# Optimization experiments

Hardware: AMD Instinct MI355X
Metric: run time of the kernel (lower is better)

The kernel has to match this reference:

```python
import jax, jax.numpy as jnp
import numpy as np

def setup_inputs() -> dict:
    key = jax.random.key(0)
    kq, kk, kv = jax.random.split(key, 3)
    S, D = 4096, 512
    q = jax.random.normal(kq, (S, D), dtype=jnp.float32)
    k = jax.random.normal(kk, (S, D), dtype=jnp.float32)
    v = jax.random.normal(kv, (S, D), dtype=jnp.float32)
    return {"q": q, "k": k, "v": v}

def reference(q, k, v):
    # scaled dot-product attention, unmasked (mask_future=False path)
    d = q.shape[-1]
    scores = jnp.einsum('sd,td->st', q, k) / jnp.sqrt(jnp.asarray(d, q.dtype))
    attn = jax.nn.softmax(scores, axis=-1)
    return jnp.einsum('st,td->sd', attn, v)
```

## Files before the change

kernel.cpp:

```cpp
#include <hip/hip_runtime.h>
#include <hip/hip_bf16.h>

#define SEQ 4096
#define DIM 512
#define SCALE 0.044194173824159216f

#define SPLITS 4
#define BQ 64
#define KVBLK 64
#define KEYS_PER_SPLIT (SEQ / SPLITS)
#define ITERS (KEYS_PER_SPLIT / KVBLK)

typedef __attribute__((ext_vector_type(8))) short short8;
typedef __attribute__((ext_vector_type(4))) float f32x4;

__device__ __forceinline__ short f2bf(float f) {
  union { float f; unsigned u; } c; c.f = f;
  unsigned u = c.u;
  return (short)((u + 0x7FFFu + ((u >> 16) & 1u)) >> 16);
}

__device__ __forceinline__ short8 pack8(float4 a, float4 b) {
  short8 r;
  r[0] = f2bf(a.x); r[1] = f2bf(a.y); r[2] = f2bf(a.z); r[3] = f2bf(a.w);
  r[4] = f2bf(b.x); r[5] = f2bf(b.y); r[6] = f2bf(b.z); r[7] = f2bf(b.w);
  return r;
}

__device__ __forceinline__ void gload16(const void* g, void* l) {
  __builtin_amdgcn_global_load_lds(
      (const __attribute__((address_space(1))) unsigned int*)g,
      (__attribute__((address_space(3))) unsigned int*)l, 16, 0, 0);
}

__global__ void cvt_bf16(const float* __restrict__ in, ushort* __restrict__ ob, int n8) {
  int i = blockIdx.x * blockDim.x + threadIdx.x;
  if (i >= n8) return;
  const float4* p = (const float4*)(in + (size_t)i * 8);
  short8 v = pack8(p[0], p[1]);
  *(short8*)(ob + (size_t)i * 8) = v;
}

__global__ void transpose_bf16(const float* __restrict__ v, ushort* __restrict__ vt) {
  __shared__ float t[64][65];
  const int bs = blockIdx.x % (SEQ / 64);
  const int bd = blockIdx.x / (SEQ / 64);
  const int s0 = bs * 64, d0 = bd * 64;
  const int tid = threadIdx.x;
#pragma unroll
  for (int k = 0; k < 16; ++k) {
    int idx = k * 256 + tid;
    int r = idx >> 6, c = idx & 63;
    t[r][c] = v[(size_t)(s0 + r) * DIM + d0 + c];
  }
  __syncthreads();
#pragma unroll
  for (int k = 0; k < 16; ++k) {
    int idx = k * 256 + tid;
    int dr = idx >> 6, sc = idx & 63;
    vt[(size_t)(d0 + dr) * SEQ + s0 + sc] = (ushort)f2bf(t[sc][dr]);
  }
}

__global__ __launch_bounds__(512) void attn_split(
    const float* __restrict__ q, const ushort* __restrict__ kbf,
    const ushort* __restrict__ vt, float* __restrict__ opart,
    float* __restrict__ ml) {
  __shared__ __align__(16) ushort kt[KVBLK * DIM];
  __shared__ __align__(16) ushort vtt[DIM * KVBLK];
  __shared__ float s_lds[BQ][68];
  __shared__ __align__(16) ushort p_lds[BQ * KVBLK];
  __shared__ float m_st[BQ], l_st[BQ], osc_st[BQ];

  const int tid  = threadIdx.x;
  const int lane = tid & 63;
  const int w    = tid >> 6;
  const int lr   = lane & 15;
  const int lg   = lane >> 4;
  const int sp   = blockIdx.x & (SPLITS - 1);
  const int qb   = blockIdx.x >> 2;
  const int rg   = w & 3;
  const int g2   = w >> 2;
  const int qrow0 = qb * BQ;
  const int kbase = sp * KEYS_PER_SPLIT;

  if (tid < BQ) { m_st[tid] = -INFINITY; l_st[tid] = 0.f; }

  short8 qf[16];
  {
    const float* qp = q + (size_t)(qrow0 + rg * 16 + lr) * DIM + lg * 8;
#pragma unroll
    for (int c = 0; c < 16; ++c)
      qf[c] = pack8(*(const float4*)(qp + c * 32), *(const float4*)(qp + c * 32 + 4));
  }
  f32x4 oacc[16] = {};

  auto stageK = [&](int kb) {
#pragma unroll
    for (int i = 0; i < 8; ++i) {
      int r = w * 8 + i;
      const ushort* src = kbf + (size_t)(kb + r) * DIM + ((lane ^ (r & 31)) * 8);
      gload16(src, &kt[r * DIM]);
    }
  };
  auto stageV = [&](int kb) {
#pragma unroll
    for (int j = 0; j < 8; ++j) {
      int r0 = w * 64 + j * 8;
      int rr = r0 + (lane >> 3);
      int c  = lane & 7;
      const ushort* src = vt + (size_t)rr * SEQ + kb + ((c ^ (rr & 7)) * 8);
      gload16(src, &vtt[r0 * KVBLK]);
    }
  };

  stageK(kbase);

  for (int it = 0; it < ITERS; ++it) {
    const int kb = kbase + it * KVBLK;

    stageV(kb);
    asm volatile("s_waitcnt vmcnt(8)" ::: "memory");
    __builtin_amdgcn_s_barrier();

    {
      f32x4 s0 = {}, s1 = {};
      const int r0 = g2 * 32 + lr;
      const int r1 = r0 + 16;
      const char* ktb = (const char*)kt;
#pragma unroll
      for (int c = 0; c < 16; ++c) {
        short8 k0 = *(const short8*)(ktb + r0 * 1024 + (((c * 4 + lg) ^ (r0 & 31)) * 16));
        short8 k1 = *(const short8*)(ktb + r1 * 1024 + (((c * 4 + lg) ^ (r1 & 31)) * 16));
        s0 = __builtin_amdgcn_mfma_f32_16x16x32_bf16(qf[c], k0, s0, 0, 0, 0);
        s1 = __builtin_amdgcn_mfma_f32_16x16x32_bf16(qf[c], k1, s1, 0, 0, 0);
      }
#pragma unroll
      for (int r = 0; r < 4; ++r) {
        s_lds[rg * 16 + lg * 4 + r][g2 * 32 + lr]      = s0[r] * SCALE;
        s_lds[rg * 16 + lg * 4 + r][g2 * 32 + 16 + lr] = s1[r] * SCALE;
      }
    }
    asm volatile("s_waitcnt lgkmcnt(0)" ::: "memory");
    __builtin_amdgcn_s_barrier();

    {
      const int srow = tid >> 3;
      const int sj   = (tid & 7) * 8;
      float4 a = *(const float4*)&s_lds[srow][sj];
      float4 b = *(const float4*)&s_lds[srow][sj + 4];
      float tmax = fmaxf(fmaxf(fmaxf(a.x, a.y), fmaxf(a.z, a.w)),
                         fmaxf(fmaxf(b.x, b.y), fmaxf(b.z, b.w)));
#pragma unroll
      for (int m = 1; m <= 4; m <<= 1) tmax = fmaxf(tmax, __shfl_xor(tmax, m));
      float mold = m_st[srow];
      float mnew = fmaxf(mold, tmax);
      float p0 = __expf(a.x - mnew), p1 = __expf(a.y - mnew);
      float p2 = __expf(a.z - mnew), p3 = __expf(a.w - mnew);
      float p4 = __expf(b.x - mnew), p5 = __expf(b.y - mnew);
      float p6 = __expf(b.z - mnew), p7 = __expf(b.w - mnew);
      float ps = ((p0 + p1) + (p2 + p3)) + ((p4 + p5) + (p6 + p7));
#pragma unroll
      for (int m = 1; m <= 4; m <<= 1) ps += __shfl_xor(ps, m);
      if ((tid & 7) == 0) {
        float sc = __expf(mold - mnew);
        osc_st[srow] = sc;
        l_st[srow] = l_st[srow] * sc + ps;
        m_st[srow] = mnew;
      }
      short8 pb;
      pb[0] = f2bf(p0); pb[1] = f2bf(p1); pb[2] = f2bf(p2); pb[3] = f2bf(p3);
      pb[4] = f2bf(p4); pb[5] = f2bf(p5); pb[6] = f2bf(p6); pb[7] = f2bf(p7);
      int ba = srow * 128 + ((sj * 2) ^ ((srow & 7) << 4));
      *(short8*)((char*)p_lds + ba) = pb;
    }

    if (it + 1 < ITERS) stageK(kb + KVBLK);

    asm volatile("s_waitcnt vmcnt(8)" ::: "memory");
    asm volatile("s_waitcnt lgkmcnt(0)" ::: "memory");
    __builtin_amdgcn_s_barrier();

    {
      float osc[4];
#pragma unroll
      for (int r = 0; r < 4; ++r) osc[r] = osc_st[rg * 16 + lg * 4 + r];
#pragma unroll
      for (int ct = 0; ct < 16; ++ct)
#pragma unroll
        for (int r = 0; r < 4; ++r) oacc[ct][r] *= osc[r];

      const char* vb = (const char*)vtt;
#pragma unroll
      for (int kc = 0; kc < 2; ++kc) {
        const int prow = rg * 16 + lr;
        int ba = prow * 128 + ((kc * 64 + lg * 16) ^ ((prow & 7) << 4));
        short8 pf = *(const short8*)((const char*)p_lds + ba);
#pragma unroll
        for (int ct = 0; ct < 16; ++ct) {
          int drow = g2 * 256 + ct * 16 + lr;
          short8 vf = *(const short8*)(vb + drow * 128 + (((kc * 4 + lg) ^ (drow & 7)) * 16));
          oacc[ct] = __builtin_amdgcn_mfma_f32_16x16x32_bf16(pf, vf, oacc[ct], 0, 0, 0);
        }
      }
    }
    asm volatile("s_waitcnt lgkmcnt(0)" ::: "memory");
    __builtin_amdgcn_s_barrier();
  }

  {
    float* op = opart + ((size_t)sp * SEQ + qrow0 + rg * 16) * DIM + g2 * 256;
#pragma unroll
    for (int ct = 0; ct < 16; ++ct)
#pragma unroll
      for (int r = 0; r < 4; ++r)
        op[(size_t)(lg * 4 + r) * DIM + ct * 16 + lr] = oacc[ct][r];
    if (tid < BQ) {
      size_t base = ((size_t)sp * SEQ + qrow0 + tid) * 2;
      ml[base]     = m_st[tid];
      ml[base + 1] = l_st[tid];
    }
  }
}

__global__ void combine(const float* __restrict__ opart, const float* __restrict__ ml,
                        float* __restrict__ out) {
  int gid = blockIdx.x * 256 + threadIdx.x;
  int row = gid >> 7;
  int dv  = (gid & 127) * 4;
  float m[SPLITS], l[SPLITS], wgt[SPLITS];
  float M = -INFINITY;
#pragma unroll
  for (int i = 0; i < SPLITS; ++i) {
    m[i] = ml[((size_t)i * SEQ + row) * 2];
    l[i] = ml[((size_t)i * SEQ + row) * 2 + 1];
    M = fmaxf(M, m[i]);
  }
  float L = 0.f;
#pragma unroll
  for (int i = 0; i < SPLITS; ++i) { wgt[i] = __expf(m[i] - M); L += l[i] * wgt[i]; }
  float inv = 1.f / L;
  float4 acc = {0.f, 0.f, 0.f, 0.f};
#pragma unroll
  for (int i = 0; i < SPLITS; ++i) {
    float4 o = *(const float4*)(opart + ((size_t)i * SEQ + row) * DIM + dv);
    acc.x += o.x * wgt[i]; acc.y += o.y * wgt[i];
    acc.z += o.z * wgt[i]; acc.w += o.w * wgt[i];
  }
  acc.x *= inv; acc.y *= inv; acc.z *= inv; acc.w *= inv;
  *(float4*)(out + (size_t)row * DIM + dv) = acc;
}

__global__ __launch_bounds__(512) void attn_fused_fb(
    const float* __restrict__ q, const float* __restrict__ k,
    const float* __restrict__ v, float* __restrict__ out) {
  __shared__ float s_lds[16][128];
  __shared__ __align__(16) unsigned short p_lds[16 * 128];
  __shared__ float m_st[16], l_st[16], osc_st[16];
  const int tid = threadIdx.x, lane = tid & 63, w = tid >> 6;
  const int lr = lane & 15, lg = lane >> 4, qb = blockIdx.x * 16;
  if (tid < 16) { m_st[tid] = -INFINITY; l_st[tid] = 0.f; }
  short8 qf[16];
  {
    const float* qp = q + (size_t)(qb + lr) * DIM + lg * 8;
#pragma unroll
    for (int c = 0; c < 16; ++c)
      qf[c] = pack8(*(const float4*)(qp + c * 32), *(const float4*)(qp + c * 32 + 4));
  }
  f32x4 oacc[4] = {};
  __syncthreads();
  for (int it = 0; it < SEQ / 128; ++it) {
    const int kb = it * 128;
    {
      const float* kp = k + (size_t)(kb + w * 16 + lr) * DIM + lg * 8;
      f32x4 sacc = {};
#pragma unroll
      for (int c = 0; c < 16; ++c) {
        short8 kf = pack8(*(const float4*)(kp + c * 32), *(const float4*)(kp + c * 32 + 4));
        sacc = __builtin_amdgcn_mfma_f32_16x16x32_bf16(qf[c], kf, sacc, 0, 0, 0);
      }
#pragma unroll
      for (int r = 0; r < 4; ++r) s_lds[lg * 4 + r][w * 16 + lr] = sacc[r] * SCALE;
    }
    __syncthreads();
    {
      const int srow = tid >> 5, sj = tid & 31;
      float4 sv = *(const float4*)&s_lds[srow][sj * 4];
      float tmax = fmaxf(fmaxf(sv.x, sv.y), fmaxf(sv.z, sv.w));
#pragma unroll
      for (int m = 16; m >= 1; m >>= 1) tmax = fmaxf(tmax, __shfl_xor(tmax, m));
      float mold = m_st[srow], mnew = fmaxf(mold, tmax);
      float p0 = __expf(sv.x - mnew), p1 = __expf(sv.y - mnew);
      float p2 = __expf(sv.z - mnew), p3 = __expf(sv.w - mnew);
      float psum = (p0 + p1) + (p2 + p3);
#pragma unroll
      for (int m = 16; m >= 1; m >>= 1) psum += __shfl_xor(psum, m);
      if (sj == 0) {
        float sc = __expf(mold - mnew);
        l_st[srow] = l_st[srow] * sc + psum; m_st[srow] = mnew; osc_st[srow] = sc;
      }
      ushort4 pb;
      pb.x = (unsigned short)f2bf(p0); pb.y = (unsigned short)f2bf(p1);
      pb.z = (unsigned short)f2bf(p2); pb.w = (unsigned short)f2bf(p3);
      int lin = srow * 256 + sj * 8;
      *(ushort4*)((char*)p_lds + (lin ^ ((srow & 7) << 4))) = pb;
    }
    __syncthreads();
    {
      float osc[4];
#pragma unroll
      for (int r = 0; r < 4; ++r) osc[r] = osc_st[lg * 4 + r];
#pragma unroll
      for (int ct = 0; ct < 4; ++ct)
#pragma unroll
        for (int r = 0; r < 4; ++r) oacc[ct][r] *= osc[r];
#pragma unroll
      for (int kc = 0; kc < 4; ++kc) {
        int lin = lr * 256 + (kc * 32 + 8 * lg) * 2;
        short8 pf = *(const short8*)((const char*)p_lds + (lin ^ ((lr & 7) << 4)));
        const float* vp0 = v + (size_t)(kb + kc * 32 + 8 * lg) * DIM + w * 64 + lr;
#pragma unroll
        for (int ct = 0; ct < 4; ++ct) {
          const float* vp = vp0 + ct * 16;
          short8 vf;
#pragma unroll
          for (int jj = 0; jj < 8; ++jj) vf[jj] = f2bf(vp[(size_t)jj * DIM]);
          oacc[ct] = __builtin_amdgcn_mfma_f32_16x16x32_bf16(pf, vf, oacc[ct], 0, 0, 0);
        }
      }
    }
    __syncthreads();
  }
  {
    float linv[4];
#pragma unroll
    for (int r = 0; r < 4; ++r) linv[r] = 1.f / l_st[lg * 4 + r];
#pragma unroll
    for (int ct = 0; ct < 4; ++ct)
#pragma unroll
      for (int r = 0; r < 4; ++r)
        out[(size_t)(qb + lg * 4 + r) * DIM + w * 64 + ct * 16 + lr] =
            oacc[ct][r] * linv[r];
  }
}

extern "C" void kernel_launch(void* const* d_in, const int* in_sizes, int n_in,
                              void* d_out, int out_size, void* d_ws, size_t ws_size,
                              hipStream_t stream) {
  (void)in_sizes; (void)n_in; (void)out_size;
  const float* q = (const float*)d_in[0];
  const float* k = (const float*)d_in[1];
  const float* v = (const float*)d_in[2];
  float* out = (float*)d_out;

  const size_t kbf_elems = (size_t)SEQ * DIM;
  const size_t vt_elems  = (size_t)DIM * SEQ;
  const size_t op_elems  = (size_t)SPLITS * SEQ * DIM;
  const size_t ml_elems  = (size_t)SPLITS * SEQ * 2;
  const size_t need = kbf_elems * 2 + vt_elems * 2 + op_elems * 4 + ml_elems * 4;

  if (ws_size >= need) {
    ushort* kbf  = (ushort*)d_ws;
    ushort* vtb  = kbf + kbf_elems;
    float* opart = (float*)(vtb + vt_elems);
    float* ml    = opart + op_elems;

    cvt_bf16<<<(SEQ * DIM / 8 + 255) / 256, 256, 0, stream>>>(k, kbf, SEQ * DIM / 8);
    transpose_bf16<<<(SEQ / 64) * (DIM / 64), 256, 0, stream>>>(v, vtb);
    attn_split<<<(SEQ / BQ) * SPLITS, 512, 0, stream>>>(q, kbf, vtb, opart, ml);
    combine<<<(SEQ * DIM / 4) / 256, 256, 0, stream>>>(opart, ml, out);
  } else {
    attn_fused_fb<<<SEQ / 16, 512, 0, stream>>>(q, k, v, out);
  }
}
```

Before: 91.58 us.

## Halve query and key tiles, split QK over head dim across warps for occupancy

```diff
diff --git a/kernel.cpp b/kernel.cpp
--- a/kernel.cpp
+++ b/kernel.cpp
@@ -6,8 +6,8 @@
 #define SCALE 0.044194173824159216f
 
 #define SPLITS 4
-#define BQ 64
-#define KVBLK 64
+#define BQ 32
+#define KVBLK 32
 #define KEYS_PER_SPLIT (SEQ / SPLITS)
 #define ITERS (KEYS_PER_SPLIT / KVBLK)
 
@@ -62,13 +62,13 @@
   }
 }
 
-__global__ __launch_bounds__(512) void attn_split(
+__global__ __launch_bounds__(512, 4) void attn_split(
     const float* __restrict__ q, const ushort* __restrict__ kbf,
     const ushort* __restrict__ vt, float* __restrict__ opart,
     float* __restrict__ ml) {
   __shared__ __align__(16) ushort kt[KVBLK * DIM];
   __shared__ __align__(16) ushort vtt[DIM * KVBLK];
-  __shared__ float s_lds[BQ][68];
+  __shared__ float s_part[2][BQ][36];
   __shared__ __align__(16) ushort p_lds[BQ * KVBLK];
   __shared__ float m_st[BQ], l_st[BQ], osc_st[BQ];
 
@@ -79,105 +79,109 @@
   const int lg   = lane >> 4;
   const int sp   = blockIdx.x & (SPLITS - 1);
   const int qb   = blockIdx.x >> 2;
-  const int rg   = w & 3;
-  const int g2   = w >> 2;
+  const int rg   = w & 1;
+  const int kg   = (w >> 1) & 1;
+  const int dh   = w >> 2;
+  const int cg   = w >> 1;
   const int qrow0 = qb * BQ;
   const int kbase = sp * KEYS_PER_SPLIT;
 
   if (tid < BQ) { m_st[tid] = -INFINITY; l_st[tid] = 0.f; }
 
-  short8 qf[16];
+  short8 qf[8];
   {
-    const float* qp = q + (size_t)(qrow0 + rg * 16 + lr) * DIM + lg * 8;
-#pragma unroll
-    for (int c = 0; c < 16; ++c)
+    const float* qp = q + (size_t)(qrow0 + rg * 16 + lr) * DIM + dh * 256 + lg * 8;
+#pragma unroll
+    for (int c = 0; c < 8; ++c)
       qf[c] = pack8(*(const float4*)(qp + c * 32), *(const float4*)(qp + c * 32 + 4));
   }
-  f32x4 oacc[16] = {};
+  f32x4 oacc[8] = {};
 
   auto stageK = [&](int kb) {
 #pragma unroll
-    for (int i = 0; i < 8; ++i) {
-      int r = w * 8 + i;
+    for (int i = 0; i < 4; ++i) {
+      int r = w * 4 + i;
       const ushort* src = kbf + (size_t)(kb + r) * DIM + ((lane ^ (r & 31)) * 8);
       gload16(src, &kt[r * DIM]);
     }
   };
   auto stageV = [&](int kb) {
 #pragma unroll
-    for (int j = 0; j < 8; ++j) {
-      int r0 = w * 64 + j * 8;
-      int rr = r0 + (lane >> 3);
-      int c  = lane & 7;
-      const ushort* src = vt + (size_t)rr * SEQ + kb + ((c ^ (rr & 7)) * 8);
+    for (int j = 0; j < 4; ++j) {
+      int r0 = w * 64 + j * 16;
+      int rr = r0 + (lane >> 2);
+      int c16 = lane & 3;
+      const ushort* src = vt + (size_t)rr * SEQ + kb + ((c16 ^ ((rr >> 1) & 3)) * 8);
       gload16(src, &vtt[r0 * KVBLK]);
     }
   };
 
   stageK(kbase);
 
+#pragma unroll 1
   for (int it = 0; it < ITERS; ++it) {
     const int kb = kbase + it * KVBLK;
 
     stageV(kb);
-    asm volatile("s_waitcnt vmcnt(8)" ::: "memory");
+    asm volatile("s_waitcnt vmcnt(4)" ::: "memory");
     __builtin_amdgcn_s_barrier();
 
     {
-      f32x4 s0 = {}, s1 = {};
-      const int r0 = g2 * 32 + lr;
-      const int r1 = r0 + 16;
-      const char* ktb = (const char*)kt;
-#pragma unroll
-      for (int c = 0; c < 16; ++c) {
-        short8 k0 = *(const short8*)(ktb + r0 * 1024 + (((c * 4 + lg) ^ (r0 & 31)) * 16));
-        short8 k1 = *(const short8*)(ktb + r1 * 1024 + (((c * 4 + lg) ^ (r1 & 31)) * 16));
-        s0 = __builtin_amdgcn_mfma_f32_16x16x32_bf16(qf[c], k0, s0, 0, 0, 0);
-        s1 = __builtin_amdgcn_mfma_f32_16x16x32_bf16(qf[c], k1, s1, 0, 0, 0);
-      }
-#pragma unroll
-      for (int r = 0; r < 4; ++r) {
-        s_lds[rg * 16 + lg * 4 + r][g2 * 32 + lr]      = s0[r] * SCALE;
-        s_lds[rg * 16 + lg * 4 + r][g2 * 32 + 16 + lr] = s1[r] * SCALE;
-      }
+      const int r0k = kg * 16 + lr;
+      const char* krow = (const char*)kt + r0k * 1024;
+      const int sw = r0k & 31;
+      f32x4 sa = {}, sb = {};
+      __builtin_amdgcn_s_setprio(1);
+#pragma unroll
+      for (int c = 0; c < 8; c += 2) {
+        short8 k0 = *(const short8*)(krow + (((dh * 32 + c * 4 + lg) ^ sw) << 4));
+        short8 k1 = *(const short8*)(krow + (((dh * 32 + (c + 1) * 4 + lg) ^ sw) << 4));
+        sa = __builtin_amdgcn_mfma_f32_16x16x32_bf16(qf[c], k0, sa, 0, 0, 0);
+        sb = __builtin_amdgcn_mfma_f32_16x16x32_bf16(qf[c + 1], k1, sb, 0, 0, 0);
+      }
+      __builtin_amdgcn_s_setprio(0);
+#pragma unroll
+      for (int r = 0; r < 4; ++r)
+        s_part[dh][rg * 16 + lg * 4 + r][kg * 16 + lr] = sa[r] + sb[r];
     }
     asm volatile("s_waitcnt lgkmcnt(0)" ::: "memory");
     __builtin_amdgcn_s_barrier();
 
     {
-      const int srow = tid >> 3;
-      const int sj   = (tid & 7) * 8;
-      float4 a = *(const float4*)&s_lds[srow][sj];
-      float4 b = *(const float4*)&s_lds[srow][sj + 4];
-      float tmax = fmaxf(fmaxf(fmaxf(a.x, a.y), fmaxf(a.z, a.w)),
-                         fmaxf(fmaxf(b.x, b.y), fmaxf(b.z, b.w)));
-#pragma unroll
-      for (int m = 1; m <= 4; m <<= 1) tmax = fmaxf(tmax, __shfl_xor(tmax, m));
+      const int srow = tid >> 4;
+      const int sjl  = tid & 15;
+      float2 a = *(const float2*)&s_part[0][srow][sjl * 2];
+      float2 b = *(const float2*)&s_part[1][srow][sjl * 2];
+      float s0 = (a.x + b.x) * SCALE;
+      float s1 = (a.y + b.y) * SCALE;
+      float tmax = fmaxf(s0, s1);
+#pragma unroll
+      for (int m = 1; m <= 8; m <<= 1) tmax = fmaxf(tmax, __shfl_xor(tmax, m));
       float mold = m_st[srow];
       float mnew = fmaxf(mold, tmax);
-      float p0 = __expf(a.x - mnew), p1 = __expf(a.y - mnew);
-      float p2 = __expf(a.z - mnew), p3 = __expf(a.w - mnew);
-      float p4 = __expf(b.x - mnew), p5 = __expf(b.y - mnew);
-      float p6 = __expf(b.z - mnew), p7 = __expf(b.w - mnew);
-      float ps = ((p0 + p1) + (p2 + p3)) + ((p4 + p5) + (p6 + p7));
-#pragma unroll
-      for (int m = 1; m <= 4; m <<= 1) ps += __shfl_xor(ps, m);
-      if ((tid & 7) == 0) {
+      float p0 = __expf(s0 - mnew), p1 = __expf(s1 - mnew);
+      float ps = p0 + p1;
+#pragma unroll
+      for (int m = 1; m <= 8; m <<= 1) ps += __shfl_xor(ps, m);
+      if (sjl == 0) {
         float sc = __expf(mold - mnew);
         osc_st[srow] = sc;
         l_st[srow] = l_st[srow] * sc + ps;
         m_st[srow] = mnew;
       }
-      short8 pb;
-      pb[0] = f2bf(p0); pb[1] = f2bf(p1); pb[2] = f2bf(p2); pb[3] = f2bf(p3);
-      pb[4] = f2bf(p4); pb[5] = f2bf(p5); pb[6] = f2bf(p6); pb[7] = f2bf(p7);
-      int ba = srow * 128 + ((sj * 2) ^ ((srow & 7) << 4));
-      *(short8*)((char*)p_lds + ba) = pb;
-    }
-
-    if (it + 1 < ITERS) stageK(kb + KVBLK);
-
-    asm volatile("s_waitcnt vmcnt(8)" ::: "memory");
+      ushort2 pb;
+      pb.x = (unsigned short)f2bf(p0);
+      pb.y = (unsigned short)f2bf(p1);
+      int ba = srow * 64 + ((sjl * 4) ^ (((srow >> 1) & 3) << 4));
+      *(ushort2*)((char*)p_lds + ba) = pb;
+    }
+
+    if (it + 1 < ITERS) {
+      stageK(kb + KVBLK);
+      asm volatile("s_waitcnt vmcnt(4)" ::: "memory");
+    } else {
+      asm volatile("s_waitcnt vmcnt(0)" ::: "memory");
+    }
     asm volatile("s_waitcnt lgkmcnt(0)" ::: "memory");
     __builtin_amdgcn_s_barrier();
 
@@ -186,32 +190,31 @@
 #pragma unroll
       for (int r = 0; r < 4; ++r) osc[r] = osc_st[rg * 16 + lg * 4 + r];
 #pragma unroll
-      for (int ct = 0; ct < 16; ++ct)
+      for (int ct = 0; ct < 8; ++ct)
 #pragma unroll
         for (int r = 0; r < 4; ++r) oacc[ct][r] *= osc[r];
 
-      const char* vb = (const char*)vtt;
-#pragma unroll
-      for (int kc = 0; kc < 2; ++kc) {
-        const int prow = rg * 16 + lr;
-        int ba = prow * 128 + ((kc * 64 + lg * 16) ^ ((prow & 7) << 4));
-        short8 pf = *(const short8*)((const char*)p_lds + ba);
-#pragma unroll
-        for (int ct = 0; ct < 16; ++ct) {
-          int drow = g2 * 256 + ct * 16 + lr;
-          short8 vf = *(const short8*)(vb + drow * 128 + (((kc * 4 + lg) ^ (drow & 7)) * 16));
-          oacc[ct] = __builtin_amdgcn_mfma_f32_16x16x32_bf16(pf, vf, oacc[ct], 0, 0, 0);
-        }
-      }
+      const int prow = rg * 16 + lr;
+      short8 pf = *(const short8*)((const char*)p_lds + prow * 64 +
+                                   ((lg ^ ((prow >> 1) & 3)) << 4));
+      const int D0 = cg * 128 + lr;
+      const char* vbase = (const char*)vtt + D0 * 64 + ((lg ^ ((D0 >> 1) & 3)) << 4);
+      __builtin_amdgcn_s_setprio(1);
+#pragma unroll
+      for (int ct = 0; ct < 8; ++ct) {
+        short8 vf = *(const short8*)(vbase + ct * 1024);
+        oacc[ct] = __builtin_amdgcn_mfma_f32_16x16x32_bf16(pf, vf, oacc[ct], 0, 0, 0);
+      }
+      __builtin_amdgcn_s_setprio(0);
     }
     asm volatile("s_waitcnt lgkmcnt(0)" ::: "memory");
     __builtin_amdgcn_s_barrier();
   }
 
   {
-    float* op = opart + ((size_t)sp * SEQ + qrow0 + rg * 16) * DIM + g2 * 256;
-#pragma unroll
-    for (int ct = 0; ct < 16; ++ct)
+    float* op = opart + ((size_t)sp * SEQ + qrow0 + rg * 16) * DIM + cg * 128;
+#pragma unroll
+    for (int ct = 0; ct < 8; ++ct)
 #pragma unroll
       for (int r = 0; r < 4; ++r)
         op[(size_t)(lg * 4 + r) * DIM + ct * 16 + lr] = oacc[ct][r];
```

Measured after the change: 107.5 us. 17.3% more time.

## Keep softmax in registers with per-wave key halves and deferred rescaling

Applied to the files above, without the earlier changes.

```diff
diff --git a/kernel.cpp b/kernel.cpp
--- a/kernel.cpp
+++ b/kernel.cpp
@@ -10,9 +10,11 @@
 #define KVBLK 64
 #define KEYS_PER_SPLIT (SEQ / SPLITS)
 #define ITERS (KEYS_PER_SPLIT / KVBLK)
+#define THR_DEFER 8.0f
 
 typedef __attribute__((ext_vector_type(8))) short short8;
 typedef __attribute__((ext_vector_type(4))) float f32x4;
+typedef __attribute__((ext_vector_type(4))) unsigned int u32x4;
 
 __device__ __forceinline__ short f2bf(float f) {
   union { float f; unsigned u; } c; c.f = f;
@@ -25,6 +27,10 @@
   r[0] = f2bf(a.x); r[1] = f2bf(a.y); r[2] = f2bf(a.z); r[3] = f2bf(a.w);
   r[4] = f2bf(b.x); r[5] = f2bf(b.y); r[6] = f2bf(b.z); r[7] = f2bf(b.w);
   return r;
+}
+
+__device__ __forceinline__ unsigned pkbf(float lo, float hi) {
+  return ((unsigned)(unsigned short)f2bf(hi) << 16) | (unsigned short)f2bf(lo);
 }
 
 __device__ __forceinline__ void gload16(const void* g, void* l) {
@@ -62,15 +68,13 @@
   }
 }
 
-__global__ __launch_bounds__(512) void attn_split(
+__global__ __launch_bounds__(512, 2) void attn_split(
     const float* __restrict__ q, const ushort* __restrict__ kbf,
     const ushort* __restrict__ vt, float* __restrict__ opart,
     float* __restrict__ ml) {
   __shared__ __align__(16) ushort kt[KVBLK * DIM];
   __shared__ __align__(16) ushort vtt[DIM * KVBLK];
-  __shared__ float s_lds[BQ][68];
-  __shared__ __align__(16) ushort p_lds[BQ * KVBLK];
-  __shared__ float m_st[BQ], l_st[BQ], osc_st[BQ];
+  __shared__ float mst[2][2][BQ];
 
   const int tid  = threadIdx.x;
   const int lane = tid & 63;
@@ -80,11 +84,9 @@
   const int sp   = blockIdx.x & (SPLITS - 1);
   const int qb   = blockIdx.x >> 2;
   const int rg   = w & 3;
-  const int g2   = w >> 2;
+  const int kh   = w >> 2;
   const int qrow0 = qb * BQ;
   const int kbase = sp * KEYS_PER_SPLIT;
-
-  if (tid < BQ) { m_st[tid] = -INFINITY; l_st[tid] = 0.f; }
 
   short8 qf[16];
   {
@@ -93,7 +95,8 @@
     for (int c = 0; c < 16; ++c)
       qf[c] = pack8(*(const float4*)(qp + c * 32), *(const float4*)(qp + c * 32 + 4));
   }
-  f32x4 oacc[16] = {};
+  f32x4 oacc[32] = {};
+  float m_reg = -INFINITY, l_reg = 0.f;
 
   auto stageK = [&](int kb) {
 #pragma unroll
@@ -108,14 +111,14 @@
     for (int j = 0; j < 8; ++j) {
       int r0 = w * 64 + j * 8;
       int rr = r0 + (lane >> 3);
-      int c  = lane & 7;
-      const ushort* src = vt + (size_t)rr * SEQ + kb + ((c ^ (rr & 7)) * 8);
+      const ushort* src = vt + (size_t)rr * SEQ + kb + (((lane & 7) ^ (rr & 7)) * 8);
       gload16(src, &vtt[r0 * KVBLK]);
     }
   };
 
   stageK(kbase);
 
+#pragma unroll 1
   for (int it = 0; it < ITERS; ++it) {
     const int kb = kbase + it * KVBLK;
 
@@ -123,102 +126,146 @@
     asm volatile("s_waitcnt vmcnt(8)" ::: "memory");
     __builtin_amdgcn_s_barrier();
 
-    {
-      f32x4 s0 = {}, s1 = {};
-      const int r0 = g2 * 32 + lr;
-      const int r1 = r0 + 16;
-      const char* ktb = (const char*)kt;
+    f32x4 s0 = {}, s1 = {};
+    {
+      const int kr0 = kh * 32 + lr;
+      const int kr1 = kr0 + 16;
+      const char* kb0 = (const char*)kt + kr0 * 1024;
+      const char* kb1 = (const char*)kt + kr1 * 1024;
+      const int sw0 = kr0 & 31, sw1 = kr1 & 31;
+      __builtin_amdgcn_s_setprio(1);
 #pragma unroll
       for (int c = 0; c < 16; ++c) {
-        short8 k0 = *(const short8*)(ktb + r0 * 1024 + (((c * 4 + lg) ^ (r0 & 31)) * 16));
-        short8 k1 = *(const short8*)(ktb + r1 * 1024 + (((c * 4 + lg) ^ (r1 & 31)) * 16));
-        s0 = __builtin_amdgcn_mfma_f32_16x16x32_bf16(qf[c], k0, s0, 0, 0, 0);
-        s1 = __builtin_amdgcn_mfma_f32_16x16x32_bf16(qf[c], k1, s1, 0, 0, 0);
-      }
+        short8 k0 = *(const short8*)(kb0 + (((c * 4 + lg) ^ sw0) << 4));
+        short8 k1 = *(const short8*)(kb1 + (((c * 4 + lg) ^ sw1) << 4));
+        s0 = __builtin_amdgcn_mfma_f32_16x16x32_bf16(k0, qf[c], s0, 0, 0, 0);
+        s1 = __builtin_amdgcn_mfma_f32_16x16x32_bf16(k1, qf[c], s1, 0, 0, 0);
+      }
+      __builtin_amdgcn_s_setprio(0);
+    }
+    __builtin_amdgcn_s_barrier();
+
+    if (it + 1 < ITERS) stageK(kb + KVBLK);
+
+    short8 pf;
+    {
+      float sc0[4], sc1[4];
+#pragma unroll
+      for (int r = 0; r < 4; ++r) { sc0[r] = s0[r] * SCALE; sc1[r] = s1[r] * SCALE; }
+      float tmax = fmaxf(fmaxf(fmaxf(sc0[0], sc0[1]), fmaxf(sc0[2], sc0[3])),
+                         fmaxf(fmaxf(sc1[0], sc1[1]), fmaxf(sc1[2], sc1[3])));
+      tmax = fmaxf(tmax, __shfl_xor(tmax, 16));
+      tmax = fmaxf(tmax, __shfl_xor(tmax, 32));
+      if (__ballot(tmax - m_reg > THR_DEFER) != 0ull) {
+        float mnew = fmaxf(m_reg, tmax);
+        float osc = __expf(m_reg - mnew);
+        m_reg = mnew;
+        l_reg *= osc;
+        float o0 = __shfl(osc, lg * 4 + 0);
+        float o1 = __shfl(osc, lg * 4 + 1);
+        float o2 = __shfl(osc, lg * 4 + 2);
+        float o3 = __shfl(osc, lg * 4 + 3);
+#pragma unroll
+        for (int ct = 0; ct < 32; ++ct) {
+          oacc[ct][0] *= o0; oacc[ct][1] *= o1;
+          oacc[ct][2] *= o2; oacc[ct][3] *= o3;
+        }
+      }
+      float p0[4], p1[4];
 #pragma unroll
       for (int r = 0; r < 4; ++r) {
-        s_lds[rg * 16 + lg * 4 + r][g2 * 32 + lr]      = s0[r] * SCALE;
-        s_lds[rg * 16 + lg * 4 + r][g2 * 32 + 16 + lr] = s1[r] * SCALE;
-      }
-    }
-    asm volatile("s_waitcnt lgkmcnt(0)" ::: "memory");
+        p0[r] = __expf(sc0[r] - m_reg);
+        p1[r] = __expf(sc1[r] - m_reg);
+      }
+      float ps = ((p0[0] + p0[1]) + (p0[2] + p0[3])) +
+                 ((p1[0] + p1[1]) + (p1[2] + p1[3]));
+      ps += __shfl_xor(ps, 16);
+      ps += __shfl_xor(ps, 32);
+      l_reg += ps;
+      unsigned d0 = pkbf(p0[0], p0[1]), d1 = pkbf(p0[2], p0[3]);
+      unsigned d2 = pkbf(p1[0], p1[1]), d3 = pkbf(p1[2], p1[3]);
+      int srcA = lr + ((lg & 1) << 5);
+      int srcB = srcA + 16;
+      unsigned xA0 = __shfl((int)d0, srcA), xA2 = __shfl((int)d2, srcA);
+      unsigned xA1 = __shfl((int)d1, srcA), xA3 = __shfl((int)d3, srcA);
+      unsigned xB0 = __shfl((int)d0, srcB), xB2 = __shfl((int)d2, srcB);
+      unsigned xB1 = __shfl((int)d1, srcB), xB3 = __shfl((int)d3, srcB);
+      bool hi = (lg >> 1) != 0;
+      union { short8 s8; u32x4 u4; } pu;
+      pu.u4[0] = hi ? xA2 : xA0;
+      pu.u4[1] = hi ? xA3 : xA1;
+      pu.u4[2] = hi ? xB2 : xB0;
+      pu.u4[3] = hi ? xB3 : xB1;
+      pf = pu.s8;
+    }
+
+    if (it + 1 < ITERS) {
+      asm volatile("s_waitcnt vmcnt(8)" ::: "memory");
+    } else {
+      asm volatile("s_waitcnt vmcnt(0)" ::: "memory");
+    }
     __builtin_amdgcn_s_barrier();
 
     {
-      const int srow = tid >> 3;
-      const int sj   = (tid & 7) * 8;
-      float4 a = *(const float4*)&s_lds[srow][sj];
-      float4 b = *(const float4*)&s_lds[srow][sj + 4];
-      float tmax = fmaxf(fmaxf(fmaxf(a.x, a.y), fmaxf(a.z, a.w)),
-                         fmaxf(fmaxf(b.x, b.y), fmaxf(b.z, b.w)));
-#pragma unroll
-      for (int m = 1; m <= 4; m <<= 1) tmax = fmaxf(tmax, __shfl_xor(tmax, m));
-      float mold = m_st[srow];
-      float mnew = fmaxf(mold, tmax);
-      float p0 = __expf(a.x - mnew), p1 = __expf(a.y - mnew);
-      float p2 = __expf(a.z - mnew), p3 = __expf(a.w - mnew);
-      float p4 = __expf(b.x - mnew), p5 = __expf(b.y - mnew);
-      float p6 = __expf(b.z - mnew), p7 = __expf(b.w - mnew);
-      float ps = ((p0 + p1) + (p2 + p3)) + ((p4 + p5) + (p6 + p7));
-#pragma unroll
-      for (int m = 1; m <= 4; m <<= 1) ps += __shfl_xor(ps, m);
-      if ((tid & 7) == 0) {
-        float sc = __expf(mold - mnew);
-        osc_st[srow] = sc;
-        l_st[srow] = l_st[srow] * sc + ps;
-        m_st[srow] = mnew;
-      }
-      short8 pb;
-      pb[0] = f2bf(p0); pb[1] = f2bf(p1); pb[2] = f2bf(p2); pb[3] = f2bf(p3);
-      pb[4] = f2bf(p4); pb[5] = f2bf(p5); pb[6] = f2bf(p6); pb[7] = f2bf(p7);
-      int ba = srow * 128 + ((sj * 2) ^ ((srow & 7) << 4));
-      *(short8*)((char*)p_lds + ba) = pb;
-    }
-
-    if (it + 1 < ITERS) stageK(kb + KVBLK);
-
-    asm volatile("s_waitcnt vmcnt(8)" ::: "memory");
-    asm volatile("s_waitcnt lgkmcnt(0)" ::: "memory");
+      __builtin_amdgcn_s_setprio(1);
+#pragma unroll
+      for (int ct = 0; ct < 32; ++ct) {
+        int vr = ct * 16 + lr;
+        short8 vf = *(const short8*)((const char*)vtt + vr * 128 +
+                                     (((kh * 4 + lg) ^ (lr & 7)) << 4));
+        oacc[ct] = __builtin_amdgcn_mfma_f32_16x16x32_bf16(pf, vf, oacc[ct], 0, 0, 0);
+      }
+      __builtin_amdgcn_s_setprio(0);
+    }
     __builtin_amdgcn_s_barrier();
-
-    {
-      float osc[4];
-#pragma unroll
-      for (int r = 0; r < 4; ++r) osc[r] = osc_st[rg * 16 + lg * 4 + r];
-#pragma unroll
-      for (int ct = 0; ct < 16; ++ct)
-#pragma unroll
-        for (int r = 0; r < 4; ++r) oacc[ct][r] *= osc[r];
-
-      const char* vb = (const char*)vtt;
-#pragma unroll
-      for (int kc = 0; kc < 2; ++kc) {
-        const int prow = rg * 16 + lr;
-        int ba = prow * 128 + ((kc * 64 + lg * 16) ^ ((prow & 7) << 4));
-        short8 pf = *(const short8*)((const char*)p_lds + ba);
-#pragma unroll
-        for (int ct = 0; ct < 16; ++ct) {
-          int drow = g2 * 256 + ct * 16 + lr;
-          short8 vf = *(const short8*)(vb + drow * 128 + (((kc * 4 + lg) ^ (drow & 7)) * 16));
-          oacc[ct] = __builtin_amdgcn_mfma_f32_16x16x32_bf16(pf, vf, oacc[ct], 0, 0, 0);
-        }
-      }
-    }
-    asm volatile("s_waitcnt lgkmcnt(0)" ::: "memory");
-    __builtin_amdgcn_s_barrier();
-  }
-
+  }
+
+  if (lane < 16) {
+    mst[kh][0][rg * 16 + lane] = m_reg;
+    mst[kh][1][rg * 16 + lane] = l_reg;
+  }
+  __syncthreads();
   {
-    float* op = opart + ((size_t)sp * SEQ + qrow0 + rg * 16) * DIM + g2 * 256;
-#pragma unroll
-    for (int ct = 0; ct < 16; ++ct)
+    float wgt[4];
+#pragma unroll
+    for (int r = 0; r < 4; ++r) {
+      int row = rg * 16 + lg * 4 + r;
+      float m0 = mst[0][0][row], m1 = mst[1][0][row];
+      float Mx = fmaxf(m0, m1);
+      wgt[r] = __expf((kh ? m1 : m0) - Mx);
+    }
+#pragma unroll
+    for (int ct = 0; ct < 32; ++ct)
+#pragma unroll
+      for (int r = 0; r < 4; ++r) oacc[ct][r] *= wgt[r];
+
+    float* stg = (rg < 2) ? (float*)kt + rg * 8192 : (float*)vtt + (rg - 2) * 8192;
+    if (kh == 1) {
+#pragma unroll
+      for (int ct = 0; ct < 32; ++ct)
+#pragma unroll
+        for (int r = 0; r < 4; ++r)
+          stg[(lg * 4 + r) * DIM + ct * 16 + lr] = oacc[ct][r];
+    }
+  }
+  __syncthreads();
+  if (kh == 0) {
+    const float* stg = (rg < 2) ? (float*)kt + rg * 8192 : (float*)vtt + (rg - 2) * 8192;
+    float* op = opart + ((size_t)sp * SEQ + qrow0 + rg * 16) * DIM;
+#pragma unroll
+    for (int ct = 0; ct < 32; ++ct)
 #pragma unroll
       for (int r = 0; r < 4; ++r)
-        op[(size_t)(lg * 4 + r) * DIM + ct * 16 + lr] = oacc[ct][r];
-    if (tid < BQ) {
-      size_t base = ((size_t)sp * SEQ + qrow0 + tid) * 2;
-      ml[base]     = m_st[tid];
-      ml[base + 1] = l_st[tid];
+        op[(size_t)(lg * 4 + r) * DIM + ct * 16 + lr] =
+            oacc[ct][r] + stg[(lg * 4 + r) * DIM + ct * 16 + lr];
+    if (lane < 16) {
+      int row = rg * 16 + lane;
+      float m0 = mst[0][0][row], m1 = mst[1][0][row];
+      float Mx = fmaxf(m0, m1);
+      float ls = mst[0][1][row] * __expf(m0 - Mx) + mst[1][1][row] * __expf(m1 - Mx);
+      size_t base = ((size_t)sp * SEQ + qrow0 + row) * 2;
+      ml[base] = Mx;
+      ml[base + 1] = ls;
     }
   }
 }
```

Result: slower. 157.1 us (+71.5%).
